# Kernel optimization log

Measured on AMD Instinct MI355X. Metric: run time of the kernel, lower is better.

Reference implementation:

```python
import jax, jax.numpy as jnp
import numpy as np

N, K, C_S, C_Z, C_G, H, NUM_RBF = 768, 32, 384, 128, 16, 4, 64
E = N * K
DH = C_Z // H  # 32
LN_EPS = 1e-5
DIST_EPS = 1e-8


def _rbf(D, D_min=0.0, D_max=20.0, D_count=NUM_RBF):
    # Gaussian radial basis expansion (GVP/ProteinMPNN style)
    mu = jnp.linspace(D_min, D_max, D_count, dtype=D.dtype)
    sigma = (D_max - D_min) / D_count
    return jnp.exp(-(((D[..., None] - mu) / sigma) ** 2))


def setup_inputs() -> dict:
    key = jax.random.key(0)
    ks = jax.random.split(key, 24)
    node_features = jax.random.normal(ks[0], (N, C_S), dtype=jnp.float32)
    node_trans = jax.random.uniform(ks[1], (N, 3), dtype=jnp.float32) * 30.0  # coords in a 30A box
    edge_features = jax.random.normal(ks[2], (E, C_Z), dtype=jnp.float32)
    src = jax.random.randint(ks[3], (E,), 0, N)
    dst = jnp.repeat(jnp.arange(N), K)  # sorted-by-destination layout (assume_sorted)
    edge_index = jnp.stack([src, dst]).astype(jnp.int64)

    def lin(k, fan_in, fan_out, scale=0.02):
        return jax.random.normal(k, (fan_in, fan_out), dtype=jnp.float32) * scale

    return {
        "node_features": node_features,
        "node_trans": node_trans,
        "edge_features": edge_features,
        "edge_index": edge_index,
        "w_left": lin(ks[4], C_S, C_G), "b_left": jnp.zeros((C_G,), jnp.float32),
        "w_right": lin(ks[5], C_S, C_G), "b_right": jnp.zeros((C_G,), jnp.float32),
        "w_bgate": lin(ks[6], C_G * C_G, C_Z), "b_bgate": jnp.zeros((C_Z,), jnp.float32),
        "w_dist": lin(ks[7], NUM_RBF, C_Z), "b_dist": jnp.zeros((C_Z,), jnp.float32),
        "w_tobias": lin(ks[8], C_Z, H),
        "ln_g": jnp.ones((C_Z,), jnp.float32), "ln_b": jnp.zeros((C_Z,), jnp.float32),
        "w_q": lin(ks[9], C_Z, C_Z), "b_q": jnp.zeros((C_Z,), jnp.float32),
        "w_kv": lin(ks[10], C_Z, 2 * C_Z), "b_kv": jnp.zeros((2 * C_Z,), jnp.float32),
        "w_out": lin(ks[11], C_Z, C_Z), "b_out": jnp.zeros((C_Z,), jnp.float32),
        "w_ogate": lin(ks[12], C_Z, C_Z), "b_ogate": jnp.zeros((C_Z,), jnp.float32),
    }


def reference(node_features, node_trans, edge_features, edge_index,
              w_left, b_left, w_right, b_right, w_bgate, b_bgate,
              w_dist, b_dist, w_tobias, ln_g, ln_b,
              w_q, b_q, w_kv, b_kv, w_out, b_out, w_ogate, b_ogate):
    # sparse -> knn graph (edges pre-sorted by destination, exactly K per node)
    knn_idx = edge_index[0].reshape(N, K)            # [N, K] source node of each neighbor edge
    feat = edge_features.reshape(N, K, C_Z)          # [N, K, c_z]

    # LayerNorm over c_z
    mu = feat.mean(-1, keepdims=True)
    var = feat.var(-1, keepdims=True)
    z = (feat - mu) * jax.lax.rsqrt(var + LN_EPS) * ln_g + ln_b  # [N, K, c_z]

    # outer-product gating bias
    nl = node_features @ w_left + b_left             # [N, c_gate_s]
    nr = node_features @ w_right + b_right
    e1 = nl[knn_idx]                                 # [N, K, c_gate_s]
    e2 = nr[knn_idx]
    edge3 = jnp.einsum('nik,njl->nijkl', e1, e2).reshape(N, K, K, C_G * C_G)
    gate = edge3 @ w_bgate + b_bgate                 # [N, K, K, c_z]

    # RBF distance bias
    t = node_trans[knn_idx]                          # [N, K, 3]
    diff = t[:, :, None, :] - t[:, None, :, :] + DIST_EPS
    dist = jnp.sqrt(jnp.sum(diff * diff, axis=-1))   # [N, K, K]
    db = _rbf(dist) @ w_dist + b_dist                # [N, K, K, c_z]
    bias = (jax.nn.sigmoid(gate) * db) @ w_tobias    # [N, K, K, H]

    # attention over the K neighbors of each node
    q = (z @ w_q + b_q).reshape(N, K, H, DH)
    kv = z @ w_kv + b_kv
    k_ = kv[..., :C_Z].reshape(N, K, H, DH)
    v = kv[..., C_Z:].reshape(N, K, H, DH)
    scores = jnp.einsum('nihd,njhd->nhij', q, k_) / jnp.sqrt(jnp.asarray(DH, q.dtype))
    scores = scores + bias.transpose(0, 3, 1, 2)     # [N, H, K, K] (mask all-True -> no -inf term)
    p = jax.nn.softmax(scores, axis=-1)
    o = jnp.einsum('nhij,njhd->nihd', p, v).reshape(N, K, C_Z)

    # output gate + projection, then knn -> sparse (identity reshape: full mask, sorted edges)
    o = o * jax.nn.sigmoid(z @ w_ogate + b_ogate)
    out = (o @ w_out + b_out).reshape(E, C_Z)
    return out
```

## Files before the change

kernel.cpp:

```cpp
#include <hip/hip_runtime.h>

#define NN   768
#define KKN  32
#define CS   384
#define CZ   128
#define CG   16
#define NH   4
#define DHD  32
#define NRBF 64
#define EE   (NN*KKN)

#define RBF_STEP    (20.0f/63.0f)
#define RBF_INVSTEP (63.0f/20.0f)
#define RBF_INVSIG  3.2f
#define RBF_SI      (RBF_STEP*RBF_INVSIG)

typedef __attribute__((ext_vector_type(8))) short bf16x8;
typedef __attribute__((ext_vector_type(4))) float f32x4;

__device__ __forceinline__ float bfl(unsigned int u){ return __uint_as_float(u << 16); }
__device__ __forceinline__ float bfh(unsigned int u){ return __uint_as_float(u & 0xFFFF0000u); }
__device__ __forceinline__ unsigned int packbf(float a, float b){
  unsigned int r;
  asm("v_cvt_pk_bf16_f32 %0, %1, %2" : "=v"(r) : "v"(a), "v"(b));
  return r;
}
__device__ __forceinline__ float fastrcp(float x){
  float r;
  asm("v_rcp_f32 %0, %1" : "=v"(r) : "v"(x));
  return r;
}
__device__ __forceinline__ float sigm(float x){ return fastrcp(1.0f + __expf(-x)); }

__global__ __launch_bounds__(256) void k1_pre(
    const float* __restrict__ nf, const float* __restrict__ ef,
    const float* __restrict__ wl, const float* __restrict__ bl,
    const float* __restrict__ wr, const float* __restrict__ br,
    const float* __restrict__ lng, const float* __restrict__ lnb,
    float* __restrict__ nlw, float* __restrict__ nrw,
    unsigned short* __restrict__ zw,
    const float* __restrict__ wq, const float* __restrict__ wkv,
    const float* __restrict__ wog, const float* __restrict__ wout,
    const float* __restrict__ wd, const float* __restrict__ wt,
    const float* __restrict__ wb, const float* __restrict__ bgf,
    unsigned short* __restrict__ wqkvogT, unsigned short* __restrict__ woutT,
    unsigned short* __restrict__ wdT, unsigned short* __restrict__ wtT,
    unsigned short* __restrict__ wbP, unsigned short* __restrict__ bgP)
{
  int b = blockIdx.x, t = threadIdx.x;
  if (b < 1536){
    int rl = t >> 4, l16 = t & 15;
    size_t e = (size_t)b*16 + rl;
    const float4* row = (const float4*)(ef + e*CZ);
    float4 x0 = row[l16*2], x1 = row[l16*2+1];
    float v[8] = {x0.x,x0.y,x0.z,x0.w,x1.x,x1.y,x1.z,x1.w};
    float s = 0.f, q = 0.f;
    #pragma unroll
    for (int u=0;u<8;u++){ s += v[u]; q += v[u]*v[u]; }
    #pragma unroll
    for (int m=1;m<16;m<<=1){ s += __shfl_xor(s,m); q += __shfl_xor(q,m); }
    float mean = s*(1.f/128.f);
    float var  = q*(1.f/128.f) - mean*mean;
    float rs = rsqrtf(var + 1e-5f);
    int c0 = l16*8;
    unsigned int pk[4];
    #pragma unroll
    for (int u=0;u<4;u++){
      float z0 = (v[2*u]  -mean)*rs*lng[c0+2*u]   + lnb[c0+2*u];
      float z1 = (v[2*u+1]-mean)*rs*lng[c0+2*u+1] + lnb[c0+2*u+1];
      pk[u] = packbf(z0,z1);
    }
    ((uint4*)(zw + e*CZ))[l16] = make_uint4(pk[0],pk[1],pk[2],pk[3]);
  } else if (b < 1920){
    int blk2 = b - 1536;
    int seg = blk2 / 96;
    int within = blk2 - seg*96;
    int gid = within*256 + t;
    int side = (gid >= 12288) ? 1 : 0;
    int idx = gid - side*12288;
    int nd = idx >> 4, c = idx & 15;
    const float* w = side ? wr : wl;
    float acc = (seg==0) ? (side ? br[c] : bl[c]) : 0.f;
    const float* nrow = nf + (size_t)nd*CS;
    int kb = seg*96;
    #pragma unroll 4
    for (int k=kb;k<kb+96;k++) acc += nrow[k]*w[k*CG+c];
    atomicAdd((side? nrw : nlw)+idx, acc);
  } else {
    int id = (b - 1920)*256 + t;
    float v[8];
    if (id < 8192){
      int c = id & 511, g = id >> 9;
      const float* src; int ld, col;
      if (c < 128){ src = wq; ld = 128; col = c; }
      else if (c < 384){ src = wkv; ld = 256; col = c-128; }
      else { src = wog; ld = 128; col = c-384; }
      #pragma unroll
      for (int j=0;j<8;j++) v[j] = src[(size_t)(g*8+j)*ld + col];
      *(uint4*)(wqkvogT + c*128 + ((g + c)&15)*8) = make_uint4(
        packbf(v[0],v[1]),packbf(v[2],v[3]),packbf(v[4],v[5]),packbf(v[6],v[7]));
    } else if (id < 10240){
      int l = id - 8192; int c = l & 127, g = l >> 7;
      #pragma unroll
      for (int j=0;j<8;j++) v[j] = wout[(size_t)(g*8+j)*128 + c];
      *(uint4*)(woutT + c*128 + ((g + c)&15)*8) = make_uint4(
        packbf(v[0],v[1]),packbf(v[2],v[3]),packbf(v[4],v[5]),packbf(v[6],v[7]));
    } else if (id < 11392){
      int l = id - 10240; int c = l & 127, g = l >> 7;
      #pragma unroll
      for (int j=0;j<8;j++) v[j] = (g<8) ? wd[(size_t)(g*8+j)*128 + c] : 0.f;
      *(uint4*)(wdT + c*72 + g*8) = make_uint4(
        packbf(v[0],v[1]),packbf(v[2],v[3]),packbf(v[4],v[5]),packbf(v[6],v[7]));
    } else if (id < 11460){
      int l = id - 11392; int h = l / 17, g = l % 17;
      #pragma unroll
      for (int j=0;j<8;j++){ int cc = g*8+j; v[j] = (cc<128)? wt[cc*4 + h] : 0.f; }
      *(uint4*)(wtT + h*136 + g*8) = make_uint4(
        packbf(v[0],v[1]),packbf(v[2],v[3]),packbf(v[4],v[5]),packbf(v[6],v[7]));
    } else if (id < 15556){
      int l2 = id - 11460;
      int c = l2 >> 5, sl = l2 & 31;
      int kl0 = sl*8;
      #pragma unroll
      for (int j=0;j<8;j++) v[j] = wb[(size_t)(kl0+j)*128 + c];
      *(uint4*)(wbP + c*256 + kl0) = make_uint4(
        packbf(v[0],v[1]),packbf(v[2],v[3]),packbf(v[4],v[5]),packbf(v[6],v[7]));
    } else if (id < 15684){
      int c = id - 15556;
      *(uint4*)(bgP + c*8) = make_uint4(packbf(bgf[c], 0.f), 0u, 0u, 0u);
    }
  }
}

__global__ __launch_bounds__(256) void k1b_sprep(
    const float* __restrict__ nlw, const float* __restrict__ nrw,
    const unsigned short* __restrict__ wbP,
    unsigned short* __restrict__ S_all, unsigned short* __restrict__ nrb)
{
  int n = blockIdx.x, t = threadIdx.x;
  float e1[16];
  #pragma unroll
  for (int k=0;k<16;k++) e1[k] = nlw[n*CG + k];
  int c = t>>1, l0 = (t&1)*8;
  float S[8];
  #pragma unroll
  for (int u=0;u<8;u++) S[u]=0.f;
  const unsigned short* wrow = wbP + c*256 + l0;
  #pragma unroll 4
  for (int k=0;k<16;k++){
    uint4 wv = *(const uint4*)(wrow + k*16);
    float wf[8] = { bfl(wv.x), bfh(wv.x), bfl(wv.y), bfh(wv.y),
                    bfl(wv.z), bfh(wv.z), bfl(wv.w), bfh(wv.w) };
    float ev = e1[k];
    #pragma unroll
    for (int u=0;u<8;u++) S[u] = fmaf(ev, wf[u], S[u]);
  }
  *(uint4*)(S_all + (size_t)n*2048 + c*16 + l0) = make_uint4(
    packbf(S[0],S[1]), packbf(S[2],S[3]), packbf(S[4],S[5]), packbf(S[6],S[7]));
  if (t < 8){
    *(unsigned int*)(nrb + n*CG + 2*t) = packbf(nrw[n*CG + 2*t], nrw[n*CG + 2*t + 1]);
  }
}

__global__ __launch_bounds__(256,4) void k2_bias(
    const long long* __restrict__ eidx, const float* __restrict__ trans,
    const unsigned short* __restrict__ S_all, const unsigned short* __restrict__ nrb,
    const unsigned short* __restrict__ wdTg, const unsigned short* __restrict__ wtTg,
    const unsigned short* __restrict__ bgP, const float* __restrict__ bd,
    float* __restrict__ biasw)
{
  int n = blockIdx.x >> 3, chunk = blockIdx.x & 7;
  int i0 = chunk*4;
  int t = threadIdx.x;
  int wave = t>>6, lane = t&63, q = lane>>4, l15 = lane&15;

  __shared__ __align__(16) unsigned short rbfb[32*72];
  __shared__ __align__(16) unsigned short Xb  [32*136];
  __shared__ __align__(16) float t3s[32][4];
  __shared__ __align__(16) float dsm[4][32];
  __shared__ int srcs[32];

  f32x4 zero4 = {0.f,0.f,0.f,0.f};
  uint4 uz = make_uint4(0,0,0,0);

  if (t < 32) srcs[t] = (int)eidx[(size_t)n*KKN + t];
  __syncthreads();
  if (t < 32){ int s = srcs[t];
    t3s[t][0]=trans[s*3]; t3s[t][1]=trans[s*3+1]; t3s[t][2]=trans[s*3+2]; }
  uint4 wdf[2][2];
  #pragma unroll
  for (int mt=0;mt<2;mt++){
    #pragma unroll
    for (int ks=0;ks<2;ks++)
      wdf[mt][ks] = *(const uint4*)(wdTg + (wave*32+mt*16+l15)*72 + ks*32 + q*8);
  }
  uint4 wtf[4];
  #pragma unroll
  for (int ks=0;ks<4;ks++)
    wtf[ks] = *(const uint4*)(wtTg + (l15&3)*136 + ks*32 + q*8);
  uint4 aBias[2];
  #pragma unroll
  for (int mt=0;mt<2;mt++)
    aBias[mt] = (q == 2) ? *(const uint4*)(bgP + (wave*32+mt*16+l15)*8) : uz;
  uint4 bE[2];
  #pragma unroll
  for (int nt=0;nt<2;nt++){
    int jn = srcs[nt*16 + l15];
    bE[nt] = (q < 2) ? *(const uint4*)(nrb + jn*CG + q*8)
                     : (q == 2 ? make_uint4(0x3F80u,0u,0u,0u) : uz);
  }
  uint4 aS[2], aSn[2];
  {
    int s0 = srcs[i0];
    #pragma unroll
    for (int mt=0;mt<2;mt++)
      aS[mt] = (q < 2) ? *(const uint4*)(S_all + (size_t)s0*2048 + (wave*32+mt*16+l15)*16 + q*8)
                       : aBias[mt];
  }
  __syncthreads();
  if (t < 128){
    int ii=t>>5, j=t&31;
    float dx=t3s[i0+ii][0]-t3s[j][0]+1e-8f;
    float dy=t3s[i0+ii][1]-t3s[j][1]+1e-8f;
    float dz=t3s[i0+ii][2]-t3s[j][2]+1e-8f;
    dsm[ii][j]=sqrtf(dx*dx+dy*dy+dz*dz);
  }
  __syncthreads();

  int jr = t>>3, sl = t&7;
  int c0base = wave*32 + q*4;
  float4 bdv[2];
  #pragma unroll
  for (int mt=0;mt<2;mt++) bdv[mt] = *(const float4*)(bd + c0base + mt*16);

  #pragma unroll 1
  for (int ii=0; ii<4; ii++){
    if (ii < 3){
      int s_n = srcs[i0+ii+1];
      #pragma unroll
      for (int mt=0;mt<2;mt++)
        aSn[mt] = (q < 2) ? *(const uint4*)(S_all + (size_t)s_n*2048 + (wave*32+mt*16+l15)*16 + q*8)
                          : aBias[mt];
    }
    {
      float dI = dsm[ii][jr]*RBF_INVSIG;
      float e[8];
      #pragma unroll
      for (int u=0;u<8;u++){
        float x = fmaf((float)(sl*8+u), -RBF_SI, dI);
        e[u] = __expf(-x*x);
      }
      *(uint4*)&rbfb[jr*72 + sl*8] = make_uint4(
        packbf(e[0],e[1]), packbf(e[2],e[3]), packbf(e[4],e[5]), packbf(e[6],e[7]));
    }
    __syncthreads();

    f32x4 ga[2][2], da[2][2];
    #pragma unroll
    for(int a=0;a<2;a++){
      #pragma unroll
      for(int b2=0;b2<2;b2++){ ga[a][b2]=zero4; da[a][b2]=zero4; }
    }
    #pragma unroll
    for(int mt=0;mt<2;mt++){
      #pragma unroll
      for(int nt=0;nt<2;nt++)
        ga[mt][nt] = __builtin_amdgcn_mfma_f32_16x16x32_bf16(
          *(const bf16x8*)&aS[mt], *(const bf16x8*)&bE[nt], ga[mt][nt], 0,0,0);
    }
    #pragma unroll
    for(int ks=0;ks<2;ks++){
      bf16x8 bR[2];
      #pragma unroll
      for(int nt=0;nt<2;nt++) bR[nt] = *(const bf16x8*)&rbfb[(nt*16+l15)*72 + ks*32 + q*8];
      #pragma unroll
      for(int mt=0;mt<2;mt++){
        #pragma unroll
        for(int nt=0;nt<2;nt++)
          da[mt][nt] = __builtin_amdgcn_mfma_f32_16x16x32_bf16(
            *(const bf16x8*)&wdf[mt][ks], bR[nt], da[mt][nt], 0,0,0);
      }
    }
    #pragma unroll
    for(int mt=0;mt<2;mt++){
      int c0 = c0base + mt*16;
      float4 bv = bdv[mt];
      #pragma unroll
      for(int nt=0;nt<2;nt++){
        float x0 = fastrcp(1.f + __expf(-ga[mt][nt][0]))*(da[mt][nt][0]+bv.x);
        float x1 = fastrcp(1.f + __expf(-ga[mt][nt][1]))*(da[mt][nt][1]+bv.y);
        float x2 = fastrcp(1.f + __expf(-ga[mt][nt][2]))*(da[mt][nt][2]+bv.z);
        float x3 = fastrcp(1.f + __expf(-ga[mt][nt][3]))*(da[mt][nt][3]+bv.w);
        *(uint2*)&Xb[(nt*16+l15)*136 + c0] = make_uint2(packbf(x0,x1), packbf(x2,x3));
      }
    }
    __syncthreads();

    if (wave < 2){
      f32x4 bacc = {0.f,0.f,0.f,0.f};
      #pragma unroll
      for(int ks=0;ks<4;ks++){
        bf16x8 bX = *(const bf16x8*)&Xb[(wave*16+l15)*136 + ks*32 + q*8];
        bacc = __builtin_amdgcn_mfma_f32_16x16x32_bf16(*(const bf16x8*)&wtf[ks], bX, bacc, 0,0,0);
      }
      if (q==0){
        int j = wave*16 + l15;
        float* base = biasw + (((size_t)n*4)*32 + (i0+ii))*32 + j;
        base[0] = bacc[0]; base[1024] = bacc[1]; base[2048] = bacc[2]; base[3072] = bacc[3];
      }
    }
    aS[0] = aSn[0]; aS[1] = aSn[1];
  }
}

__global__ __launch_bounds__(256,3) void k3_attn(
    const unsigned short* __restrict__ zw, const float* __restrict__ biasw,
    const unsigned short* __restrict__ wqkvogT, const unsigned short* __restrict__ woutT,
    const float* __restrict__ bq, const float* __restrict__ bkv, const float* __restrict__ bog,
    const float* __restrict__ bout, float* __restrict__ out)
{
  int n = blockIdx.x, t = threadIdx.x;
  int w = t>>6, lane = t&63, q = lane>>4, l15 = lane&15;
  int i3 = lane>>1, jh = lane&1;

  __shared__ __align__(16) char smem[49152];
  uint4* wdst = (uint4*)(smem + 32768);
  unsigned short* wtS = (unsigned short*)(smem + 32768);
  f32x4 zero4 = {0.f,0.f,0.f,0.f};

  bf16x8 zfr[2][4];
  #pragma unroll
  for (int nt=0;nt<2;nt++){
    const unsigned short* zr = zw + ((size_t)n*32 + nt*16 + l15)*128;
    #pragma unroll
    for (int ks=0;ks<4;ks++) zfr[nt][ks] = *(const bf16x8*)(zr + ks*32 + q*8);
  }
  f32x4 br4[4];
  {
    const f32x4* bsrc = (const f32x4*)(biasw + (((size_t)n*4 + w)*32 + i3)*32 + jh*16);
    #pragma unroll
    for (int u=0;u<4;u++) br4[u] = bsrc[u];
  }
  const float* bseg = (w==0)? bq : (w==1)? bkv : (w==2)? (bkv+128) : bog;

  const uint4* wsrc = (const uint4*)wqkvogT;
  int sb = w*2048, db = w*256;
  uint4 sreg[4];
  #pragma unroll
  for (int u=0;u<4;u++) sreg[u] = wsrc[sb + u*64 + lane];
  const unsigned short* arow = wtS + w*2048 + l15*128;
  for (int r=0;r<8;r++){
    #pragma unroll
    for (int u=0;u<4;u++) wdst[db + u*64 + lane] = sreg[u];
    if (r<7){
      #pragma unroll
      for (int u=0;u<4;u++) sreg[u] = wsrc[sb + (r+1)*256 + u*64 + lane];
    }
    float4 bv = *(const float4*)(bseg + r*16 + q*4);
    f32x4 acc0 = zero4, acc1 = zero4;
    int cg = w*128 + r*16 + l15;
    #pragma unroll
    for (int ks=0;ks<4;ks++){
      bf16x8 af = *(const bf16x8*)(arow + (((ks*4+q) + cg)&15)*8);
      acc0 = __builtin_amdgcn_mfma_f32_16x16x32_bf16(af, zfr[0][ks], acc0, 0,0,0);
      acc1 = __builtin_amdgcn_mfma_f32_16x16x32_bf16(af, zfr[1][ks], acc1, 0,0,0);
    }
    #pragma unroll
    for (int nt=0;nt<2;nt++){
      f32x4 a = nt? acc1 : acc0;
      float v0,v1,v2,v3;
      if (w==3){ v0=sigm(a[0]+bv.x); v1=sigm(a[1]+bv.y); v2=sigm(a[2]+bv.z); v3=sigm(a[3]+bv.w); }
      else     { v0=a[0]+bv.x; v1=a[1]+bv.y; v2=a[2]+bv.z; v3=a[3]+bv.w; }
      int i = nt*16 + l15;
      int blk = ((r*2 + (q>>1)) + i) & 15;
      *(uint2*)(smem + w*8192 + i*256 + blk*16 + (q&1)*8) = make_uint2(packbf(v0,v1), packbf(v2,v3));
    }
  }
  __syncthreads();

  float sc[16];
  {
    float qreg[32];
    #pragma unroll
    for (int dq=0;dq<4;dq++){
      uint4 qa = *(const uint4*)(smem + i3*256 + (((w*4+dq) + i3)&15)*16);
      unsigned int qu[4] = {qa.x,qa.y,qa.z,qa.w};
      #pragma unroll
      for (int u2=0;u2<4;u2++){ qreg[dq*8+2*u2]=bfl(qu[u2]); qreg[dq*8+2*u2+1]=bfh(qu[u2]); }
    }
    int j0 = jh*16;
    #pragma unroll
    for (int jj=0;jj<16;jj++){
      int j = j0+jj;
      float s = 0.f;
      #pragma unroll
      for (int dq=0;dq<4;dq++){
        uint4 ka = *(const uint4*)(smem + 8192 + j*256 + (((w*4+dq) + j)&15)*16);
        unsigned int ku[4] = {ka.x,ka.y,ka.z,ka.w};
        #pragma unroll
        for (int u2=0;u2<4;u2++)
          s += qreg[dq*8+2*u2]*bfl(ku[u2]) + qreg[dq*8+2*u2+1]*bfh(ku[u2]);
      }
      sc[jj] = s*0.17677669529663687f + br4[jj>>2][jj&3];
    }
  }
  {
    float mx = sc[0];
    #pragma unroll
    for (int jj=1;jj<16;jj++) mx = fmaxf(mx, sc[jj]);
    mx = fmaxf(mx, __shfl_xor(mx,1));
    float sum = 0.f;
    #pragma unroll
    for (int jj=0;jj<16;jj++){ sc[jj] = __expf(sc[jj]-mx); sum += sc[jj]; }
    sum += __shfl_xor(sum,1);
    float inv = fastrcp(sum);
    #pragma unroll
    for (int jj=0;jj<16;jj++) sc[jj] *= inv;
  }
  __syncthreads();
  {
    int dbase = w*32 + jh*16;
    int db8 = dbase >> 3;
    float o16[16];
    #pragma unroll
    for (int u=0;u<16;u++) o16[u]=0.f;
    #pragma unroll
    for (int j=0;j<32;j++){
      float pj = __shfl(sc[j & 15], (lane & 62) | (j >> 4));
      uint4 va0 = *(const uint4*)(smem + 16384 + j*256 + (((db8+0) + j)&15)*16);
      uint4 va1 = *(const uint4*)(smem + 16384 + j*256 + (((db8+1) + j)&15)*16);
      unsigned int vu[8] = {va0.x,va0.y,va0.z,va0.w,va1.x,va1.y,va1.z,va1.w};
      #pragma unroll
      for (int u2=0;u2<8;u2++){ o16[2*u2] += pj*bfl(vu[u2]); o16[2*u2+1] += pj*bfh(vu[u2]); }
    }
    uint4 ga0 = *(const uint4*)(smem + 24576 + i3*256 + (((db8+0) + i3)&15)*16);
    uint4 ga1 = *(const uint4*)(smem + 24576 + i3*256 + (((db8+1) + i3)&15)*16);
    unsigned int gu[8] = {ga0.x,ga0.y,ga0.z,ga0.w,ga1.x,ga1.y,ga1.z,ga1.w};
    #pragma unroll
    for (int u2=0;u2<8;u2++){
      float y0 = o16[2*u2]  *bfl(gu[u2]);
      float y1 = o16[2*u2+1]*bfh(gu[u2]);
      int c = dbase + 2*u2;
      *(unsigned int*)(smem + i3*256 + (((c>>3) + i3)&15)*16 + (c&7)*2) = packbf(y0,y1);
    }
  }
  __syncthreads();

  bf16x8 yfr[2][4];
  #pragma unroll
  for (int mt=0;mt<2;mt++){
    int row = mt*16 + l15;
    #pragma unroll
    for (int ks=0;ks<4;ks++)
      yfr[mt][ks] = *(const bf16x8*)(smem + row*256 + (((ks*4+q) + row)&15)*16);
  }
  const uint4* osrc = (const uint4*)woutT;
  #pragma unroll
  for (int r2=0;r2<2;r2++){
    int c0 = (r2*4 + w)*16;
    #pragma unroll
    for (int u=0;u<4;u++) wdst[db + u*64 + lane] = osrc[c0*16 + u*64 + lane];
    int cg2 = c0 + l15;
    const unsigned short* brow = wtS + w*2048 + l15*128;
    f32x4 oa0 = zero4, oa1 = zero4;
    #pragma unroll
    for (int ks=0;ks<4;ks++){
      bf16x8 bf = *(const bf16x8*)(brow + (((ks*4+q) + cg2)&15)*8);
      oa0 = __builtin_amdgcn_mfma_f32_16x16x32_bf16(yfr[0][ks], bf, oa0, 0,0,0);
      oa1 = __builtin_amdgcn_mfma_f32_16x16x32_bf16(yfr[1][ks], bf, oa1, 0,0,0);
    }
    float bov = bout[cg2];
    #pragma unroll
    for (int mt=0;mt<2;mt++){
      f32x4 oa = mt? oa1 : oa0;
      #pragma unroll
      for (int rg=0; rg<4; rg++){
        int i = mt*16 + q*4 + rg;
        out[((size_t)n*32 + i)*128 + cg2] = oa[rg] + bov;
      }
    }
  }
}

extern "C" void kernel_launch(void* const* d_in, const int* in_sizes, int n_in,
                              void* d_out, int out_size, void* d_ws, size_t ws_size,
                              hipStream_t stream)
{
  const float* nf  = (const float*)d_in[0];
  const float* tr  = (const float*)d_in[1];
  const float* ef  = (const float*)d_in[2];
  const long long* ei = (const long long*)d_in[3];
  const float* wl  = (const float*)d_in[4];  const float* bl  = (const float*)d_in[5];
  const float* wr  = (const float*)d_in[6];  const float* br  = (const float*)d_in[7];
  const float* wbg = (const float*)d_in[8];  const float* bbg = (const float*)d_in[9];
  const float* wdi = (const float*)d_in[10]; const float* bdi = (const float*)d_in[11];
  const float* wtb = (const float*)d_in[12];
  const float* lng = (const float*)d_in[13]; const float* lnb = (const float*)d_in[14];
  const float* wq  = (const float*)d_in[15]; const float* bq  = (const float*)d_in[16];
  const float* wkv = (const float*)d_in[17]; const float* bkv = (const float*)d_in[18];
  const float* wo  = (const float*)d_in[19]; const float* bo  = (const float*)d_in[20];
  const float* wog = (const float*)d_in[21]; const float* bog = (const float*)d_in[22];
  float* outp = (float*)d_out;
  float* ws = (float*)d_ws;
  float* nlw = ws;
  float* nrw = ws + 12288;
  float* biasw = ws + 24576;
  unsigned short* zw      = (unsigned short*)(ws + 3170304);
  unsigned short* wqkvogT = (unsigned short*)(ws + 4743168);
  unsigned short* woutT   = (unsigned short*)(ws + 4775936);
  unsigned short* wdTg    = (unsigned short*)(ws + 4784128);
  unsigned short* wtTg    = (unsigned short*)(ws + 4788736);
  unsigned short* bgPg    = wtTg + 544;
  unsigned short* wbPg    = (unsigned short*)(ws + 4789824);
  unsigned short* S_all   = (unsigned short*)(ws + 4806208);
  unsigned short* nrb     = (unsigned short*)(ws + 5592640);

  hipMemsetAsync(nlw, 0, 24576*sizeof(float), stream);
  hipLaunchKernelGGL(k1_pre, dim3(1982), dim3(256), 0, stream,
                     nf, ef, wl, bl, wr, br, lng, lnb, nlw, nrw, zw,
                     wq, wkv, wog, wo, wdi, wtb, wbg, bbg,
                     wqkvogT, woutT, wdTg, wtTg, wbPg, bgPg);
  hipLaunchKernelGGL(k1b_sprep, dim3(768), dim3(256), 0, stream,
                     nlw, nrw, wbPg, S_all, nrb);
  hipLaunchKernelGGL(k2_bias, dim3(6144), dim3(256), 0, stream,
                     ei, tr, S_all, nrb, wdTg, wtTg, bgPg, bdi, biasw);
  hipLaunchKernelGGL(k3_attn, dim3(768), dim3(256), 0, stream,
                     zw, biasw, wqkvogT, woutT, bq, bkv, bog, bo, outp);
}
```

Before: 218.5 us.

## Use MFMA for attention QK and PV, split node projection finer

The attention kernel now computes the Q·K scores and P·V products with bf16 MFMA instructions instead of scalar dot-product loops. V is stored transposed in shared memory and the softmax probabilities are written to LDS as bf16. The row softmax now uses cross-lane shuffles and normalisation is applied after P·V. Separately, the node left/right projection uses eight 48-wide K segments instead of four, giving more atomic-add blocks, and the RBF compute in k2 is moved before the next-iteration prefetch. Rounding P to bf16 adds precision loss, and the extra segments double the atomics.

```diff
diff --git a/kernel.cpp b/kernel.cpp
--- a/kernel.cpp
+++ b/kernel.cpp
@@ -71,7 +71,7 @@
       pk[u] = packbf(z0,z1);
     }
     ((uint4*)(zw + e*CZ))[l16] = make_uint4(pk[0],pk[1],pk[2],pk[3]);
-  } else if (b < 1920){
+  } else if (b < 2304){
     int blk2 = b - 1536;
     int seg = blk2 / 96;
     int within = blk2 - seg*96;
@@ -82,12 +82,12 @@
     const float* w = side ? wr : wl;
     float acc = (seg==0) ? (side ? br[c] : bl[c]) : 0.f;
     const float* nrow = nf + (size_t)nd*CS;
-    int kb = seg*96;
+    int kb = seg*48;
     #pragma unroll 4
-    for (int k=kb;k<kb+96;k++) acc += nrow[k]*w[k*CG+c];
+    for (int k=kb;k<kb+48;k++) acc += nrow[k]*w[k*CG+c];
     atomicAdd((side? nrw : nlw)+idx, acc);
   } else {
-    int id = (b - 1920)*256 + t;
+    int id = (b - 2304)*256 + t;
     float v[8];
     if (id < 8192){
       int c = id & 511, g = id >> 9;
@@ -235,23 +235,23 @@
 
   #pragma unroll 1
   for (int ii=0; ii<4; ii++){
+    {
+      float dI = dsm[ii][jr]*RBF_INVSIG;
+      float e[8];
+      #pragma unroll
+      for (int u=0;u<8;u++){
+        float x = fmaf((float)(sl*8+u), -RBF_SI, dI);
+        e[u] = __expf(-x*x);
+      }
+      *(uint4*)&rbfb[jr*72 + sl*8] = make_uint4(
+        packbf(e[0],e[1]), packbf(e[2],e[3]), packbf(e[4],e[5]), packbf(e[6],e[7]));
+    }
     if (ii < 3){
       int s_n = srcs[i0+ii+1];
       #pragma unroll
       for (int mt=0;mt<2;mt++)
         aSn[mt] = (q < 2) ? *(const uint4*)(S_all + (size_t)s_n*2048 + (wave*32+mt*16+l15)*16 + q*8)
                           : aBias[mt];
-    }
-    {
-      float dI = dsm[ii][jr]*RBF_INVSIG;
-      float e[8];
-      #pragma unroll
-      for (int u=0;u<8;u++){
-        float x = fmaf((float)(sl*8+u), -RBF_SI, dI);
-        e[u] = __expf(-x*x);
-      }
-      *(uint4*)&rbfb[jr*72 + sl*8] = make_uint4(
-        packbf(e[0],e[1]), packbf(e[2],e[3]), packbf(e[4],e[5]), packbf(e[6],e[7]));
     }
     __syncthreads();
 
@@ -321,7 +321,6 @@
 {
   int n = blockIdx.x, t = threadIdx.x;
   int w = t>>6, lane = t&63, q = lane>>4, l15 = lane&15;
-  int i3 = lane>>1, jh = lane&1;
 
   __shared__ __align__(16) char smem[49152];
   uint4* wdst = (uint4*)(smem + 32768);
@@ -334,12 +333,6 @@
     const unsigned short* zr = zw + ((size_t)n*32 + nt*16 + l15)*128;
     #pragma unroll
     for (int ks=0;ks<4;ks++) zfr[nt][ks] = *(const bf16x8*)(zr + ks*32 + q*8);
-  }
-  f32x4 br4[4];
-  {
-    const f32x4* bsrc = (const f32x4*)(biasw + (((size_t)n*4 + w)*32 + i3)*32 + jh*16);
-    #pragma unroll
-    for (int u=0;u<4;u++) br4[u] = bsrc[u];
   }
   const float* bseg = (w==0)? bq : (w==1)? bkv : (w==2)? (bkv+128) : bog;
 
@@ -372,76 +365,107 @@
       if (w==3){ v0=sigm(a[0]+bv.x); v1=sigm(a[1]+bv.y); v2=sigm(a[2]+bv.z); v3=sigm(a[3]+bv.w); }
       else     { v0=a[0]+bv.x; v1=a[1]+bv.y; v2=a[2]+bv.z; v3=a[3]+bv.w; }
       int i = nt*16 + l15;
-      int blk = ((r*2 + (q>>1)) + i) & 15;
-      *(uint2*)(smem + w*8192 + i*256 + blk*16 + (q&1)*8) = make_uint2(packbf(v0,v1), packbf(v2,v3));
+      if (w==2){
+        unsigned short* vt = (unsigned short*)(smem + 16384) + (r*16 + q*4)*32 + i;
+        unsigned int u01 = packbf(v0,v1), u23 = packbf(v2,v3);
+        vt[0]  = (unsigned short)u01;  vt[32] = (unsigned short)(u01>>16);
+        vt[64] = (unsigned short)u23;  vt[96] = (unsigned short)(u23>>16);
+      } else {
+        int blk = ((r*2 + (q>>1)) + i) & 15;
+        *(uint2*)(smem + w*8192 + i*256 + blk*16 + (q&1)*8) = make_uint2(packbf(v0,v1), packbf(v2,v3));
+      }
     }
   }
   __syncthreads();
 
-  float sc[16];
+  f32x4 sc4[2][2];
   {
-    float qreg[32];
-    #pragma unroll
-    for (int dq=0;dq<4;dq++){
-      uint4 qa = *(const uint4*)(smem + i3*256 + (((w*4+dq) + i3)&15)*16);
-      unsigned int qu[4] = {qa.x,qa.y,qa.z,qa.w};
-      #pragma unroll
-      for (int u2=0;u2<4;u2++){ qreg[dq*8+2*u2]=bfl(qu[u2]); qreg[dq*8+2*u2+1]=bfh(qu[u2]); }
-    }
-    int j0 = jh*16;
-    #pragma unroll
-    for (int jj=0;jj<16;jj++){
-      int j = j0+jj;
-      float s = 0.f;
-      #pragma unroll
-      for (int dq=0;dq<4;dq++){
-        uint4 ka = *(const uint4*)(smem + 8192 + j*256 + (((w*4+dq) + j)&15)*16);
-        unsigned int ku[4] = {ka.x,ka.y,ka.z,ka.w};
-        #pragma unroll
-        for (int u2=0;u2<4;u2++)
-          s += qreg[dq*8+2*u2]*bfl(ku[u2]) + qreg[dq*8+2*u2+1]*bfh(ku[u2]);
-      }
-      sc[jj] = s*0.17677669529663687f + br4[jj>>2][jj&3];
-    }
-  }
+    uint4 aQ[2], bK[2];
+    #pragma unroll
+    for (int mt=0;mt<2;mt++){
+      int row = mt*16 + l15;
+      aQ[mt] = *(const uint4*)(smem + row*256 + (((w*4+q) + row)&15)*16);
+    }
+    #pragma unroll
+    for (int nt=0;nt<2;nt++){
+      int row = nt*16 + l15;
+      bK[nt] = *(const uint4*)(smem + 8192 + row*256 + (((w*4+q) + row)&15)*16);
+    }
+    #pragma unroll
+    for (int mt=0;mt<2;mt++){
+      #pragma unroll
+      for (int nt=0;nt<2;nt++)
+        sc4[mt][nt] = __builtin_amdgcn_mfma_f32_16x16x32_bf16(
+          *(const bf16x8*)&aQ[mt], *(const bf16x8*)&bK[nt], zero4, 0,0,0);
+    }
+  }
+  const float* bb = biasw + (size_t)(n*4 + w)*1024;
+  float inv_[2][4];
+  #pragma unroll
+  for (int mt=0;mt<2;mt++){
+    #pragma unroll
+    for (int rg=0;rg<4;rg++){
+      int i = mt*16 + q*4 + rg;
+      sc4[mt][0][rg] = fmaf(sc4[mt][0][rg], 0.17677669529663687f, bb[i*32 + l15]);
+      sc4[mt][1][rg] = fmaf(sc4[mt][1][rg], 0.17677669529663687f, bb[i*32 + 16 + l15]);
+      float m = fmaxf(sc4[mt][0][rg], sc4[mt][1][rg]);
+      m = fmaxf(m, __shfl_xor(m,1));
+      m = fmaxf(m, __shfl_xor(m,2));
+      m = fmaxf(m, __shfl_xor(m,4));
+      m = fmaxf(m, __shfl_xor(m,8));
+      sc4[mt][0][rg] = __expf(sc4[mt][0][rg] - m);
+      sc4[mt][1][rg] = __expf(sc4[mt][1][rg] - m);
+      float s = sc4[mt][0][rg] + sc4[mt][1][rg];
+      s += __shfl_xor(s,1); s += __shfl_xor(s,2);
+      s += __shfl_xor(s,4); s += __shfl_xor(s,8);
+      inv_[mt][rg] = fastrcp(s);
+    }
+  }
+  unsigned short* Pl = (unsigned short*)(smem + 32768 + w*4096);
+  #pragma unroll
+  for (int mt=0;mt<2;mt++){
+    #pragma unroll
+    for (int nt=0;nt<2;nt++){
+      unsigned int u01 = packbf(sc4[mt][nt][0], sc4[mt][nt][1]);
+      unsigned int u23 = packbf(sc4[mt][nt][2], sc4[mt][nt][3]);
+      unsigned short* pp = Pl + (mt*16 + q*4)*32 + nt*16 + l15;
+      pp[0]  = (unsigned short)u01;  pp[32] = (unsigned short)(u01>>16);
+      pp[64] = (unsigned short)u23;  pp[96] = (unsigned short)(u23>>16);
+    }
+  }
+  __syncthreads();
+
+  f32x4 ov[2][2];
   {
-    float mx = sc[0];
-    #pragma unroll
-    for (int jj=1;jj<16;jj++) mx = fmaxf(mx, sc[jj]);
-    mx = fmaxf(mx, __shfl_xor(mx,1));
-    float sum = 0.f;
-    #pragma unroll
-    for (int jj=0;jj<16;jj++){ sc[jj] = __expf(sc[jj]-mx); sum += sc[jj]; }
-    sum += __shfl_xor(sum,1);
-    float inv = fastrcp(sum);
-    #pragma unroll
-    for (int jj=0;jj<16;jj++) sc[jj] *= inv;
-  }
-  __syncthreads();
-  {
-    int dbase = w*32 + jh*16;
-    int db8 = dbase >> 3;
-    float o16[16];
-    #pragma unroll
-    for (int u=0;u<16;u++) o16[u]=0.f;
-    #pragma unroll
-    for (int j=0;j<32;j++){
-      float pj = __shfl(sc[j & 15], (lane & 62) | (j >> 4));
-      uint4 va0 = *(const uint4*)(smem + 16384 + j*256 + (((db8+0) + j)&15)*16);
-      uint4 va1 = *(const uint4*)(smem + 16384 + j*256 + (((db8+1) + j)&15)*16);
-      unsigned int vu[8] = {va0.x,va0.y,va0.z,va0.w,va1.x,va1.y,va1.z,va1.w};
-      #pragma unroll
-      for (int u2=0;u2<8;u2++){ o16[2*u2] += pj*bfl(vu[u2]); o16[2*u2+1] += pj*bfh(vu[u2]); }
-    }
-    uint4 ga0 = *(const uint4*)(smem + 24576 + i3*256 + (((db8+0) + i3)&15)*16);
-    uint4 ga1 = *(const uint4*)(smem + 24576 + i3*256 + (((db8+1) + i3)&15)*16);
-    unsigned int gu[8] = {ga0.x,ga0.y,ga0.z,ga0.w,ga1.x,ga1.y,ga1.z,ga1.w};
-    #pragma unroll
-    for (int u2=0;u2<8;u2++){
-      float y0 = o16[2*u2]  *bfl(gu[u2]);
-      float y1 = o16[2*u2+1]*bfh(gu[u2]);
-      int c = dbase + 2*u2;
-      *(unsigned int*)(smem + i3*256 + (((c>>3) + i3)&15)*16 + (c&7)*2) = packbf(y0,y1);
+    uint4 aP[2], bV[2];
+    #pragma unroll
+    for (int mt=0;mt<2;mt++)
+      aP[mt] = *(const uint4*)(Pl + (mt*16 + l15)*32 + q*8);
+    #pragma unroll
+    for (int nt2=0;nt2<2;nt2++)
+      bV[nt2] = *(const uint4*)((unsigned short*)(smem + 16384) + (w*32 + nt2*16 + l15)*32 + q*8);
+    #pragma unroll
+    for (int mt=0;mt<2;mt++){
+      #pragma unroll
+      for (int nt2=0;nt2<2;nt2++)
+        ov[mt][nt2] = __builtin_amdgcn_mfma_f32_16x16x32_bf16(
+          *(const bf16x8*)&aP[mt], *(const bf16x8*)&bV[nt2], zero4, 0,0,0);
+    }
+  }
+  #pragma unroll
+  for (int mt=0;mt<2;mt++){
+    #pragma unroll
+    for (int nt2=0;nt2<2;nt2++){
+      #pragma unroll
+      for (int rg=0;rg<4;rg++){
+        int i = mt*16 + q*4 + rg;
+        int c = w*32 + nt2*16 + l15;
+        int off = i*256 + (((c>>3) + i)&15)*16 + (c&7)*2;
+        unsigned short gus = *(const unsigned short*)(smem + 24576 + off);
+        float g = __uint_as_float(((unsigned int)gus) << 16);
+        float yv = ov[mt][nt2][rg] * inv_[mt][rg] * g;
+        *(unsigned short*)(smem + off) = (unsigned short)packbf(yv, yv);
+      }
     }
   }
   __syncthreads();
@@ -516,7 +540,7 @@
   unsigned short* nrb     = (unsigned short*)(ws + 5592640);
 
   hipMemsetAsync(nlw, 0, 24576*sizeof(float), stream);
-  hipLaunchKernelGGL(k1_pre, dim3(1982), dim3(256), 0, stream,
+  hipLaunchKernelGGL(k1_pre, dim3(2366), dim3(256), 0, stream,
                      nf, ef, wl, bl, wr, br, lng, lnb, nlw, nrw, zw,
                      wq, wkv, wog, wo, wdi, wtb, wbg, bbg,
                      wqkvogT, woutT, wdTg, wtTg, wbPg, bgPg);
```

Result: faster. 211.8 us (-3.0%).
